# Performance work log

Measured on AMD Instinct MI355X. Metric: run time of the kernel, lower is better.

The kernel has to match this reference:

```python
import jax, jax.numpy as jnp
import numpy as np

N, DIM, DK, DV = 8192, 512, 128, 128


def setup_inputs() -> dict:
    key = jax.random.key(0)
    ks = jax.random.split(key, 6)
    s = lambda d: 1.0 / np.sqrt(d)
    return {
        "x": jax.random.normal(ks[0], (N, DIM), jnp.float32),
        "W": jax.random.normal(ks[1], (DK, DIM), jnp.float32) * s(DIM),
        "b": jax.random.normal(ks[2], (DK,), jnp.float32) * s(DIM),
        "Wv": jax.random.normal(ks[3], (DV, DIM), jnp.float32) * s(DIM),
        "bv": jax.random.normal(ks[4], (DV,), jnp.float32) * s(DIM),
        "a": jax.random.normal(ks[5], (2 * DK,), jnp.float32),
    }


def reference(x, W, b, Wv, bv, a):
    dk = a.shape[0] // 2
    wx = x @ W.T + b                      # [n, dk]
    # additive GAT score decomposed into two matvecs + outer sum
    s_src = wx @ a[:dk]                   # [n]
    s_dst = wx @ a[dk:]                   # [n]
    score = s_src[:, None] + s_dst[None, :]  # [n, n]
    score = jax.nn.leaky_relu(score, negative_slope=0.01)
    score = jax.nn.softmax(score, axis=-1)
    v = x @ Wv.T + bv                     # [n, dv]
    return score @ v                      # [n, dv]
```

## Files before the change

kernel.cpp:

```cpp
#include <hip/hip_runtime.h>
#include <math.h>

static constexpr int N    = 8192;
static constexpr int DIM  = 512;
static constexpr int DK   = 128;
static constexpr int DV   = 128;
static constexpr float SLOPE = 0.01f;

static constexpr int NCH  = 512;
static constexpr int CHSZ = 16;
static constexpr int NCOL = 258;

static constexpr int MT  = 128;
static constexpr int BK  = 32;
static constexpr int LDT = 132;

__global__ __launch_bounds__(256) void k_front(const float* __restrict__ x,
                                               const float* __restrict__ W,
                                               const float* __restrict__ b,
                                               const float* __restrict__ a,
                                               float* __restrict__ s_src,
                                               float* __restrict__ s_dst) {
    __shared__ float sa[2 * DK];
    __shared__ float sus[DIM + 32], sud[DIM + 32];
    __shared__ float sc[2];
    int tid = threadIdx.x;
    sa[tid] = a[tid];
    __syncthreads();

    {
        float p = 0.0f;
        if (tid < 64)        p = b[tid] * sa[tid] + b[tid + 64] * sa[tid + 64];
        else if (tid < 128) { int l = tid - 64; p = b[l] * sa[DK + l] + b[l + 64] * sa[DK + 64 + l]; }
#pragma unroll
        for (int off = 32; off > 0; off >>= 1) p += __shfl_down(p, off);
        if (tid == 0)  sc[0] = p;
        if (tid == 64) sc[1] = p;
    }

#pragma unroll
    for (int half = 0; half < 2; ++half) {
        int d = tid + half * 256;
        float us = 0.0f, ud = 0.0f;
#pragma unroll 4
        for (int k = 0; k < DK; ++k) {
            float w = W[(size_t)k * DIM + d];
            us += w * sa[k];
            ud += w * sa[DK + k];
        }
        int dp = d + (d >> 6) * 4;
        sus[dp] = us;
        sud[dp] = ud;
    }
    __syncthreads();

    int r   = tid >> 3;
    int seg = tid & 7;
    int row = blockIdx.x * 32 + r;
    const float* xr = x + (size_t)row * DIM;
    int base  = seg * 64;
    int baseP = base + seg * 4;
    float accs = 0.0f, accd = 0.0f;
#pragma unroll
    for (int i = 0; i < 16; ++i) {
        float4 q  = *reinterpret_cast<const float4*>(xr + base + i * 4);
        float4 u4 = *reinterpret_cast<const float4*>(&sus[baseP + i * 4]);
        float4 w4 = *reinterpret_cast<const float4*>(&sud[baseP + i * 4]);
        accs += q.x * u4.x + q.y * u4.y + q.z * u4.z + q.w * u4.w;
        accd += q.x * w4.x + q.y * w4.y + q.z * w4.z + q.w * w4.w;
    }
#pragma unroll
    for (int off = 4; off > 0; off >>= 1) {
        accs += __shfl_down(accs, off);
        accd += __shfl_down(accd, off);
    }
    if (seg == 0) {
        s_src[row] = accs + sc[0];
        s_dst[row] = accd + sc[1];
    }
}

__global__ __launch_bounds__(256) void k_v(const float* __restrict__ x,
                                           const float* __restrict__ Wv,
                                           float* __restrict__ vpart, int ksplit) {
    __shared__ float At[BK][LDT];
    __shared__ float Bt[BK][LDT];
    int tid = threadIdx.x;
    int mt  = blockIdx.x & 63;
    int ks  = blockIdx.x >> 6;
    int row0 = mt * MT;
    int ksub = DIM / ksplit;
    int kb0  = ks * ksub;
    int nt   = ksub / BK;
    int tx = tid & 15, ty = tid >> 4;

    float acc[8][8];
#pragma unroll
    for (int i = 0; i < 8; ++i)
#pragma unroll
        for (int j = 0; j < 8; ++j) acc[i][j] = 0.0f;

    int fr[4], fk[4];
#pragma unroll
    for (int i = 0; i < 4; ++i) {
        int f = tid + i * 256;
        fr[i] = f >> 3;
        fk[i] = (f & 7) * 4;
    }
    float4 px[4], pw[4];
#pragma unroll
    for (int i = 0; i < 4; ++i) {
        px[i] = *reinterpret_cast<const float4*>(x  + (size_t)(row0 + fr[i]) * DIM + kb0 + fk[i]);
        pw[i] = *reinterpret_cast<const float4*>(Wv + (size_t)fr[i] * DIM + kb0 + fk[i]);
    }

    for (int t = 0; t < nt; ++t) {
#pragma unroll
        for (int i = 0; i < 4; ++i) {
            At[fk[i] + 0][fr[i]] = px[i].x;
            At[fk[i] + 1][fr[i]] = px[i].y;
            At[fk[i] + 2][fr[i]] = px[i].z;
            At[fk[i] + 3][fr[i]] = px[i].w;
            Bt[fk[i] + 0][fr[i]] = pw[i].x;
            Bt[fk[i] + 1][fr[i]] = pw[i].y;
            Bt[fk[i] + 2][fr[i]] = pw[i].z;
            Bt[fk[i] + 3][fr[i]] = pw[i].w;
        }
        __syncthreads();
        if (t < nt - 1) {
            int kb = kb0 + (t + 1) * BK;
#pragma unroll
            for (int i = 0; i < 4; ++i) {
                px[i] = *reinterpret_cast<const float4*>(x  + (size_t)(row0 + fr[i]) * DIM + kb + fk[i]);
                pw[i] = *reinterpret_cast<const float4*>(Wv + (size_t)fr[i] * DIM + kb + fk[i]);
            }
        }
#pragma unroll 4
        for (int kk = 0; kk < BK; ++kk) {
            float4 a0 = *reinterpret_cast<const float4*>(&At[kk][ty * 4]);
            float4 a1 = *reinterpret_cast<const float4*>(&At[kk][64 + ty * 4]);
            float4 b0 = *reinterpret_cast<const float4*>(&Bt[kk][tx * 4]);
            float4 b1 = *reinterpret_cast<const float4*>(&Bt[kk][64 + tx * 4]);
            float av[8] = {a0.x, a0.y, a0.z, a0.w, a1.x, a1.y, a1.z, a1.w};
            float bw[8] = {b0.x, b0.y, b0.z, b0.w, b1.x, b1.y, b1.z, b1.w};
#pragma unroll
            for (int i = 0; i < 8; ++i)
#pragma unroll
                for (int j = 0; j < 8; ++j) acc[i][j] += av[i] * bw[j];
        }
        __syncthreads();
    }

#pragma unroll
    for (int rh = 0; rh < 2; ++rh)
#pragma unroll
        for (int i = 0; i < 4; ++i) {
            int row = row0 + rh * 64 + ty * 4 + i;
            float* dst = vpart + ((size_t)ks * N + row) * DV;
#pragma unroll
            for (int ch = 0; ch < 2; ++ch) {
                float4 o;
                o.x = acc[rh * 4 + i][ch * 4 + 0];
                o.y = acc[rh * 4 + i][ch * 4 + 1];
                o.z = acc[rh * 4 + i][ch * 4 + 2];
                o.w = acc[rh * 4 + i][ch * 4 + 3];
                *reinterpret_cast<float4*>(dst + ch * 64 + tx * 4) = o;
            }
        }
}

__global__ __launch_bounds__(256) void k_rank_scatter(const float* __restrict__ s_dst,
                                                      float* __restrict__ d_sorted,
                                                      int* __restrict__ perm) {
    __shared__ __align__(16) float sd[N];
    __shared__ int part[256];
    int tid = threadIdx.x;
    for (int t = tid; t < N / 4; t += 256)
        reinterpret_cast<float4*>(sd)[t] = reinterpret_cast<const float4*>(s_dst)[t];
    __syncthreads();
    int j0  = blockIdx.x * 16;
    int jj  = tid >> 4;
    int seg = tid & 15;
    int j   = j0 + jj;
    float dj = sd[j];
    int cnt = 0;
    const float4* sdv = reinterpret_cast<const float4*>(sd);
    for (int c = 0; c < 128; ++c) {
        int f4 = c * 16 + seg;
        float4 q = sdv[f4];
        int i0 = f4 * 4;
        cnt += (q.x < dj || (q.x == dj && (i0 + 0) < j));
        cnt += (q.y < dj || (q.y == dj && (i0 + 1) < j));
        cnt += (q.z < dj || (q.z == dj && (i0 + 2) < j));
        cnt += (q.w < dj || (q.w == dj && (i0 + 3) < j));
    }
    part[tid] = cnt;
    __syncthreads();
    if (tid < 16) {
        int s = 0;
#pragma unroll
        for (int t = 0; t < 16; ++t) s += part[tid * 16 + t];
        int jw = j0 + tid;
        d_sorted[s] = sd[jw];
        perm[s] = jw;
    }
}

__global__ __launch_bounds__(256) void k_vredY(const float* __restrict__ vpart,
                                               const float* __restrict__ bv,
                                               const float* __restrict__ d_sorted,
                                               const int* __restrict__ perm,
                                               float* __restrict__ Y1,
                                               float* __restrict__ Y2,
                                               double* __restrict__ chunk_tot,
                                               int ksplit) {
    __shared__ float sv[CHSZ][DV];
    __shared__ float se1[CHSZ], se2[CHSZ];
    int ch  = blockIdx.x;
    int tid = threadIdx.x;
    int g   = tid >> 5;
    int c4  = tid & 31;
    float dmax = d_sorted[N - 1];
    if (tid < CHSZ) {
        float d = d_sorted[ch * CHSZ + tid];
        se1[tid] = expf(d - dmax);
        se2[tid] = expf(SLOPE * d);
    }
    __syncthreads();
    float4 bb = reinterpret_cast<const float4*>(bv)[c4];
#pragma unroll
    for (int half = 0; half < 2; ++half) {
        int rl = half * 8 + g;
        int r  = ch * CHSZ + rl;
        int j  = perm[r];
        float4 s = {0.f, 0.f, 0.f, 0.f};
        for (int ksp = 0; ksp < ksplit; ++ksp) {
            float4 q = *reinterpret_cast<const float4*>(vpart + ((size_t)ksp * N + j) * DV + c4 * 4);
            s.x += q.x; s.y += q.y; s.z += q.z; s.w += q.w;
        }
        s.x += bb.x; s.y += bb.y; s.z += bb.z; s.w += bb.w;
        *reinterpret_cast<float4*>(&sv[rl][c4 * 4]) = s;
        float e1 = se1[rl], e2 = se2[rl];
        float4 o1 = {e1 * s.x, e1 * s.y, e1 * s.z, e1 * s.w};
        float4 o2 = {e2 * s.x, e2 * s.y, e2 * s.z, e2 * s.w};
        *reinterpret_cast<float4*>(Y1 + (size_t)r * DV + c4 * 4) = o1;
        *reinterpret_cast<float4*>(Y2 + (size_t)r * DV + c4 * 4) = o2;
    }
    __syncthreads();
    int col = tid & 127;
    bool is2 = tid >= 128;
    double acc = 0.0;
#pragma unroll
    for (int k = 0; k < CHSZ; ++k) {
        float e = is2 ? se2[k] : se1[k];
        acc += (double)(e * sv[k][col]);
    }
    chunk_tot[(size_t)ch * NCOL + tid] = acc;
    if (tid == 0) {
        double z = 0.0;
#pragma unroll
        for (int k = 0; k < CHSZ; ++k) z += (double)se1[k];
        chunk_tot[(size_t)ch * NCOL + 256] = z;
    }
    if (tid == 1) {
        double z = 0.0;
#pragma unroll
        for (int k = 0; k < CHSZ; ++k) z += (double)se2[k];
        chunk_tot[(size_t)ch * NCOL + 257] = z;
    }
}

__global__ __launch_bounds__(256) void k_coff(const double* __restrict__ chunk_tot,
                                              double* __restrict__ chunk_off,
                                              double* __restrict__ totals) {
    __shared__ double sp[256];
    int col = blockIdx.x;
    int tid = threadIdx.x;
    double v0 = chunk_tot[(size_t)(2 * tid) * NCOL + col];
    double v1 = chunk_tot[(size_t)(2 * tid + 1) * NCOL + col];
    double p = v0 + v1;
    sp[tid] = p;
    __syncthreads();
    for (int off = 1; off < 256; off <<= 1) {
        double t = (tid >= off) ? sp[tid - off] : 0.0;
        __syncthreads();
        sp[tid] += t;
        __syncthreads();
    }
    double excl = sp[tid] - p;
    chunk_off[(size_t)(2 * tid) * NCOL + col]     = excl;
    chunk_off[(size_t)(2 * tid + 1) * NCOL + col] = excl + v0;
    if (tid == 255) totals[col] = sp[255];
}

__global__ __launch_bounds__(256) void k_scanW(const float* __restrict__ Y1,
                                               const float* __restrict__ Y2,
                                               const float* __restrict__ d_sorted,
                                               const double* __restrict__ chunk_off,
                                               float* __restrict__ P1,
                                               float* __restrict__ P2,
                                               double* __restrict__ pz1,
                                               double* __restrict__ pz2) {
    int ch  = blockIdx.x;
    int tid = threadIdx.x;
    int col = tid & 127;
    bool is2 = tid >= 128;
    const float* Y = is2 ? Y2 : Y1;
    float* P       = is2 ? P2 : P1;
    double acc = chunk_off[(size_t)ch * NCOL + tid];
#pragma unroll
    for (int k = 0; k < CHSZ; ++k) {
        size_t idx = (size_t)(ch * CHSZ + k) * DV + col;
        P[idx] = (float)acc;
        acc += (double)Y[idx];
    }
    if (tid < 2) {
        float dmax = d_sorted[N - 1];
        double z = chunk_off[(size_t)ch * NCOL + 256 + tid];
        double* pz = tid == 0 ? pz1 : pz2;
#pragma unroll
        for (int k = 0; k < CHSZ; ++k) {
            int r = ch * CHSZ + k;
            float d = d_sorted[r];
            float e = (tid == 0) ? expf(d - dmax) : expf(SLOPE * d);
            pz[r] = z;
            z += (double)e;
        }
    }
}

__global__ __launch_bounds__(256) void k_final(const float* __restrict__ s_src,
                                               const float* __restrict__ d_sorted,
                                               const float* __restrict__ P1,
                                               const float* __restrict__ P2,
                                               const double* __restrict__ pz1,
                                               const double* __restrict__ pz2,
                                               const double* __restrict__ totals,
                                               float* __restrict__ out) {
    __shared__ int ski[8];
    __shared__ float ssi[8];
    int tid = threadIdx.x;
    int rbase = blockIdx.x * 8;
    if (tid < 8) {
        int row = rbase + tid;
        float si = s_src[row];
        float thr = -si;
        int lo = 0, hi = N;
        while (lo < hi) {
            int mid = (lo + hi) >> 1;
            if (d_sorted[mid] <= thr) lo = mid + 1; else hi = mid;
        }
        ski[tid] = lo;
        ssi[tid] = si;
    }
    __syncthreads();
    float dmax = d_sorted[N - 1];
    int dv = tid & 127;
    int half = tid >> 7;
    double T1 = totals[dv];
    double T2 = totals[128 + dv];
    double z1T = totals[256], z2T = totals[257];
#pragma unroll
    for (int it = 0; it < 4; ++it) {
        int r2 = it * 2 + half;
        int row = rbase + r2;
        float si = ssi[r2];
        int ki = ski[r2];
        float t = si + dmax;
        float m = t > 0.0f ? t : SLOPE * t;
        float alpha = expf(t - m);
        float beta  = expf(SLOPE * si - m);
        double suf1, sufz1, pre2, prez2;
        if (ki < N) {
            suf1  = T1 - (double)P1[(size_t)ki * DV + dv];
            sufz1 = z1T - pz1[ki];
            pre2  = (double)P2[(size_t)ki * DV + dv];
            prez2 = pz2[ki];
        } else {
            suf1 = 0.0; sufz1 = 0.0; pre2 = T2; prez2 = z2T;
        }
        double num = (double)alpha * suf1  + (double)beta * pre2;
        double den = (double)alpha * sufz1 + (double)beta * prez2;
        out[(size_t)row * DV + dv] = (float)(num / den);
    }
}

extern "C" void kernel_launch(void* const* d_in, const int* in_sizes, int n_in,
                              void* d_out, int out_size, void* d_ws, size_t ws_size,
                              hipStream_t stream) {
    const float* x  = (const float*)d_in[0];
    const float* W  = (const float*)d_in[1];
    const float* b  = (const float*)d_in[2];
    const float* Wv = (const float*)d_in[3];
    const float* bv = (const float*)d_in[4];
    const float* a  = (const float*)d_in[5];
    float* out = (float*)d_out;

    char* base = (char*)d_ws;
    size_t off = 0;
    auto carve = [&](size_t bytes) -> void* {
        void* p = base + off;
        off = (off + bytes + 255) & ~(size_t)255;
        return p;
    };
    float*  s_src     = (float*)carve(N * sizeof(float));
    float*  s_dst     = (float*)carve(N * sizeof(float));
    float*  d_sorted  = (float*)carve(N * sizeof(float));
    int*    perm      = (int*)carve(N * sizeof(int));
    double* pz1       = (double*)carve(N * sizeof(double));
    double* pz2       = (double*)carve(N * sizeof(double));
    double* chunk_tot = (double*)carve((size_t)NCH * NCOL * sizeof(double));
    double* chunk_off = (double*)carve((size_t)NCH * NCOL * sizeof(double));
    double* totals    = (double*)carve(NCOL * sizeof(double));
    float*  Y1        = (float*)carve((size_t)N * DV * sizeof(float));
    float*  Y2        = (float*)carve((size_t)N * DV * sizeof(float));

    const size_t planeB = (size_t)N * DV * sizeof(float);
    size_t avail = ws_size > off ? ws_size - off : 0;
    int ksplit = 2;
    if (avail >= 8 * planeB + 4096)      ksplit = 8;
    else if (avail >= 4 * planeB + 4096) ksplit = 4;
    if (ksplit == 8) ksplit = 4;
    size_t unionBytes = (size_t)(ksplit > 2 ? ksplit : 2) * planeB;
    char* uni = (char*)carve(unionBytes);
    float* vpart = (float*)uni;
    float* P1    = (float*)uni;
    float* P2    = (float*)(uni + planeB);

    k_front<<<N / 32, 256, 0, stream>>>(x, W, b, a, s_src, s_dst);
    k_v<<<64 * ksplit, 256, 0, stream>>>(x, Wv, vpart, ksplit);
    k_rank_scatter<<<N / 16, 256, 0, stream>>>(s_dst, d_sorted, perm);
    k_vredY<<<NCH, 256, 0, stream>>>(vpart, bv, d_sorted, perm, Y1, Y2, chunk_tot, ksplit);
    k_coff<<<NCOL, 256, 0, stream>>>(chunk_tot, chunk_off, totals);
    k_scanW<<<NCH, 256, 0, stream>>>(Y1, Y2, d_sorted, chunk_off, P1, P2, pz1, pz2);
    k_final<<<N / 8, 256, 0, stream>>>(s_src, d_sorted, P1, P2, pz1, pz2, totals, out);
}
```

Measured before the change: 160.1 us.

## Fuse score front-end with V GEMM and recompute V gather instead of storing Y planes

Merges the score-projection kernel and the split-K V GEMM into one launch whose blocks branch by index, so the two independent stages share the GPU. It also drops the Y1/Y2 intermediate planes: the scan kernel re-gathers and reduces vpart for each chunk and applies the exp weights itself, instead of reading stored weighted values. This removes one launch and two full N×DV write-and-read passes, at the cost of gathering and reducing vpart twice and a larger shared-memory footprint in the fused kernel.

```diff
diff --git a/kernel.cpp b/kernel.cpp
--- a/kernel.cpp
+++ b/kernel.cpp
@@ -14,6 +14,175 @@
 static constexpr int MT  = 128;
 static constexpr int BK  = 32;
 static constexpr int LDT = 132;
+static constexpr int KSPLIT = 4;
+static constexpr int KSUB   = DIM / KSPLIT;
+
+__device__ __forceinline__ void gemm_body(int mt, int ks, int ksub, int tid,
+                                          const float* __restrict__ x,
+                                          const float* __restrict__ Wv,
+                                          float* __restrict__ vpart,
+                                          float (*At)[LDT], float (*Bt)[LDT]) {
+    int row0 = mt * MT;
+    int kb0  = ks * ksub;
+    int nt   = ksub / BK;
+    int tx = tid & 15, ty = tid >> 4;
+
+    float acc[8][8];
+#pragma unroll
+    for (int i = 0; i < 8; ++i)
+#pragma unroll
+        for (int j = 0; j < 8; ++j) acc[i][j] = 0.0f;
+
+    int fr[4], fk[4];
+#pragma unroll
+    for (int i = 0; i < 4; ++i) {
+        int f = tid + i * 256;
+        fr[i] = f >> 3;
+        fk[i] = (f & 7) * 4;
+    }
+    float4 px[4], pw[4];
+#pragma unroll
+    for (int i = 0; i < 4; ++i) {
+        px[i] = *reinterpret_cast<const float4*>(x  + (size_t)(row0 + fr[i]) * DIM + kb0 + fk[i]);
+        pw[i] = *reinterpret_cast<const float4*>(Wv + (size_t)fr[i] * DIM + kb0 + fk[i]);
+    }
+
+    for (int t = 0; t < nt; ++t) {
+#pragma unroll
+        for (int i = 0; i < 4; ++i) {
+            At[fk[i] + 0][fr[i]] = px[i].x;
+            At[fk[i] + 1][fr[i]] = px[i].y;
+            At[fk[i] + 2][fr[i]] = px[i].z;
+            At[fk[i] + 3][fr[i]] = px[i].w;
+            Bt[fk[i] + 0][fr[i]] = pw[i].x;
+            Bt[fk[i] + 1][fr[i]] = pw[i].y;
+            Bt[fk[i] + 2][fr[i]] = pw[i].z;
+            Bt[fk[i] + 3][fr[i]] = pw[i].w;
+        }
+        __syncthreads();
+        if (t < nt - 1) {
+            int kb = kb0 + (t + 1) * BK;
+#pragma unroll
+            for (int i = 0; i < 4; ++i) {
+                px[i] = *reinterpret_cast<const float4*>(x  + (size_t)(row0 + fr[i]) * DIM + kb + fk[i]);
+                pw[i] = *reinterpret_cast<const float4*>(Wv + (size_t)fr[i] * DIM + kb + fk[i]);
+            }
+        }
+#pragma unroll 4
+        for (int kk = 0; kk < BK; ++kk) {
+            float4 a0 = *reinterpret_cast<const float4*>(&At[kk][ty * 4]);
+            float4 a1 = *reinterpret_cast<const float4*>(&At[kk][64 + ty * 4]);
+            float4 b0 = *reinterpret_cast<const float4*>(&Bt[kk][tx * 4]);
+            float4 b1 = *reinterpret_cast<const float4*>(&Bt[kk][64 + tx * 4]);
+            float av[8] = {a0.x, a0.y, a0.z, a0.w, a1.x, a1.y, a1.z, a1.w};
+            float bw[8] = {b0.x, b0.y, b0.z, b0.w, b1.x, b1.y, b1.z, b1.w};
+#pragma unroll
+            for (int i = 0; i < 8; ++i)
+#pragma unroll
+                for (int j = 0; j < 8; ++j) acc[i][j] += av[i] * bw[j];
+        }
+        __syncthreads();
+    }
+
+#pragma unroll
+    for (int rh = 0; rh < 2; ++rh)
+#pragma unroll
+        for (int i = 0; i < 4; ++i) {
+            int row = row0 + rh * 64 + ty * 4 + i;
+            float* dst = vpart + ((size_t)ks * N + row) * DV;
+#pragma unroll
+            for (int ch = 0; ch < 2; ++ch) {
+                float4 o;
+                o.x = acc[rh * 4 + i][ch * 4 + 0];
+                o.y = acc[rh * 4 + i][ch * 4 + 1];
+                o.z = acc[rh * 4 + i][ch * 4 + 2];
+                o.w = acc[rh * 4 + i][ch * 4 + 3];
+                *reinterpret_cast<float4*>(dst + ch * 64 + tx * 4) = o;
+            }
+        }
+}
+
+__device__ __forceinline__ void front_body(int fb, int tid,
+                                           const float* __restrict__ x,
+                                           const float* __restrict__ W,
+                                           const float* __restrict__ b,
+                                           const float* __restrict__ a,
+                                           float* __restrict__ s_src,
+                                           float* __restrict__ s_dst,
+                                           float* sa, float* sus, float* sud, float* sc) {
+    sa[tid] = a[tid];
+    __syncthreads();
+    {
+        float p = 0.0f;
+        if (tid < 64)        p = b[tid] * sa[tid] + b[tid + 64] * sa[tid + 64];
+        else if (tid < 128) { int l = tid - 64; p = b[l] * sa[DK + l] + b[l + 64] * sa[DK + 64 + l]; }
+#pragma unroll
+        for (int off = 32; off > 0; off >>= 1) p += __shfl_down(p, off);
+        if (tid == 0)  sc[0] = p;
+        if (tid == 64) sc[1] = p;
+    }
+#pragma unroll
+    for (int half = 0; half < 2; ++half) {
+        int d = tid + half * 256;
+        float us = 0.0f, ud = 0.0f;
+#pragma unroll 4
+        for (int k = 0; k < DK; ++k) {
+            float w = W[(size_t)k * DIM + d];
+            us += w * sa[k];
+            ud += w * sa[DK + k];
+        }
+        int dp = d + (d >> 6) * 4;
+        sus[dp] = us;
+        sud[dp] = ud;
+    }
+    __syncthreads();
+    int r   = tid >> 3;
+    int seg = tid & 7;
+    int row = fb * 32 + r;
+    const float* xr = x + (size_t)row * DIM;
+    int base  = seg * 64;
+    int baseP = base + seg * 4;
+    float accs = 0.0f, accd = 0.0f;
+#pragma unroll
+    for (int i = 0; i < 16; ++i) {
+        float4 q  = *reinterpret_cast<const float4*>(xr + base + i * 4);
+        float4 u4 = *reinterpret_cast<const float4*>(&sus[baseP + i * 4]);
+        float4 w4 = *reinterpret_cast<const float4*>(&sud[baseP + i * 4]);
+        accs += q.x * u4.x + q.y * u4.y + q.z * u4.z + q.w * u4.w;
+        accd += q.x * w4.x + q.y * w4.y + q.z * w4.z + q.w * w4.w;
+    }
+#pragma unroll
+    for (int off = 4; off > 0; off >>= 1) {
+        accs += __shfl_down(accs, off);
+        accd += __shfl_down(accd, off);
+    }
+    if (seg == 0) {
+        s_src[row] = accs + sc[0];
+        s_dst[row] = accd + sc[1];
+    }
+}
+
+__global__ __launch_bounds__(256) void k_frontv(const float* __restrict__ x,
+                                                const float* __restrict__ W,
+                                                const float* __restrict__ b,
+                                                const float* __restrict__ a,
+                                                const float* __restrict__ Wv,
+                                                float* __restrict__ s_src,
+                                                float* __restrict__ s_dst,
+                                                float* __restrict__ vpart) {
+    __shared__ float At[BK][LDT];
+    __shared__ float Bt[BK][LDT];
+    __shared__ float sa[2 * DK];
+    __shared__ float sus[DIM + 32], sud[DIM + 32];
+    __shared__ float sc[2];
+    int blk = blockIdx.x;
+    int tid = threadIdx.x;
+    if (blk < 256) {
+        gemm_body(blk & 63, blk >> 6, KSUB, tid, x, Wv, vpart, At, Bt);
+    } else {
+        front_body(blk - 256, tid, x, W, b, a, s_src, s_dst, sa, sus, sud, sc);
+    }
+}
 
 __global__ __launch_bounds__(256) void k_front(const float* __restrict__ x,
                                                const float* __restrict__ W,
@@ -24,60 +193,7 @@
     __shared__ float sa[2 * DK];
     __shared__ float sus[DIM + 32], sud[DIM + 32];
     __shared__ float sc[2];
-    int tid = threadIdx.x;
-    sa[tid] = a[tid];
-    __syncthreads();
-
-    {
-        float p = 0.0f;
-        if (tid < 64)        p = b[tid] * sa[tid] + b[tid + 64] * sa[tid + 64];
-        else if (tid < 128) { int l = tid - 64; p = b[l] * sa[DK + l] + b[l + 64] * sa[DK + 64 + l]; }
-#pragma unroll
-        for (int off = 32; off > 0; off >>= 1) p += __shfl_down(p, off);
-        if (tid == 0)  sc[0] = p;
-        if (tid == 64) sc[1] = p;
-    }
-
-#pragma unroll
-    for (int half = 0; half < 2; ++half) {
-        int d = tid + half * 256;
-        float us = 0.0f, ud = 0.0f;
-#pragma unroll 4
-        for (int k = 0; k < DK; ++k) {
-            float w = W[(size_t)k * DIM + d];
-            us += w * sa[k];
-            ud += w * sa[DK + k];
-        }
-        int dp = d + (d >> 6) * 4;
-        sus[dp] = us;
-        sud[dp] = ud;
-    }
-    __syncthreads();
-
-    int r   = tid >> 3;
-    int seg = tid & 7;
-    int row = blockIdx.x * 32 + r;
-    const float* xr = x + (size_t)row * DIM;
-    int base  = seg * 64;
-    int baseP = base + seg * 4;
-    float accs = 0.0f, accd = 0.0f;
-#pragma unroll
-    for (int i = 0; i < 16; ++i) {
-        float4 q  = *reinterpret_cast<const float4*>(xr + base + i * 4);
-        float4 u4 = *reinterpret_cast<const float4*>(&sus[baseP + i * 4]);
-        float4 w4 = *reinterpret_cast<const float4*>(&sud[baseP + i * 4]);
-        accs += q.x * u4.x + q.y * u4.y + q.z * u4.z + q.w * u4.w;
-        accd += q.x * w4.x + q.y * w4.y + q.z * w4.z + q.w * w4.w;
-    }
-#pragma unroll
-    for (int off = 4; off > 0; off >>= 1) {
-        accs += __shfl_down(accs, off);
-        accd += __shfl_down(accd, off);
-    }
-    if (seg == 0) {
-        s_src[row] = accs + sc[0];
-        s_dst[row] = accd + sc[1];
-    }
+    front_body(blockIdx.x, threadIdx.x, x, W, b, a, s_src, s_dst, sa, sus, sud, sc);
 }
 
 __global__ __launch_bounds__(256) void k_v(const float* __restrict__ x,
@@ -85,88 +201,7 @@
                                            float* __restrict__ vpart, int ksplit) {
     __shared__ float At[BK][LDT];
     __shared__ float Bt[BK][LDT];
-    int tid = threadIdx.x;
-    int mt  = blockIdx.x & 63;
-    int ks  = blockIdx.x >> 6;
-    int row0 = mt * MT;
-    int ksub = DIM / ksplit;
-    int kb0  = ks * ksub;
-    int nt   = ksub / BK;
-    int tx = tid & 15, ty = tid >> 4;
-
-    float acc[8][8];
-#pragma unroll
-    for (int i = 0; i < 8; ++i)
-#pragma unroll
-        for (int j = 0; j < 8; ++j) acc[i][j] = 0.0f;
-
-    int fr[4], fk[4];
-#pragma unroll
-    for (int i = 0; i < 4; ++i) {
-        int f = tid + i * 256;
-        fr[i] = f >> 3;
-        fk[i] = (f & 7) * 4;
-    }
-    float4 px[4], pw[4];
-#pragma unroll
-    for (int i = 0; i < 4; ++i) {
-        px[i] = *reinterpret_cast<const float4*>(x  + (size_t)(row0 + fr[i]) * DIM + kb0 + fk[i]);
-        pw[i] = *reinterpret_cast<const float4*>(Wv + (size_t)fr[i] * DIM + kb0 + fk[i]);
-    }
-
-    for (int t = 0; t < nt; ++t) {
-#pragma unroll
-        for (int i = 0; i < 4; ++i) {
-            At[fk[i] + 0][fr[i]] = px[i].x;
-            At[fk[i] + 1][fr[i]] = px[i].y;
-            At[fk[i] + 2][fr[i]] = px[i].z;
-            At[fk[i] + 3][fr[i]] = px[i].w;
-            Bt[fk[i] + 0][fr[i]] = pw[i].x;
-            Bt[fk[i] + 1][fr[i]] = pw[i].y;
-            Bt[fk[i] + 2][fr[i]] = pw[i].z;
-            Bt[fk[i] + 3][fr[i]] = pw[i].w;
-        }
-        __syncthreads();
-        if (t < nt - 1) {
-            int kb = kb0 + (t + 1) * BK;
-#pragma unroll
-            for (int i = 0; i < 4; ++i) {
-                px[i] = *reinterpret_cast<const float4*>(x  + (size_t)(row0 + fr[i]) * DIM + kb + fk[i]);
-                pw[i] = *reinterpret_cast<const float4*>(Wv + (size_t)fr[i] * DIM + kb + fk[i]);
-            }
-        }
-#pragma unroll 4
-        for (int kk = 0; kk < BK; ++kk) {
-            float4 a0 = *reinterpret_cast<const float4*>(&At[kk][ty * 4]);
-            float4 a1 = *reinterpret_cast<const float4*>(&At[kk][64 + ty * 4]);
-            float4 b0 = *reinterpret_cast<const float4*>(&Bt[kk][tx * 4]);
-            float4 b1 = *reinterpret_cast<const float4*>(&Bt[kk][64 + tx * 4]);
-            float av[8] = {a0.x, a0.y, a0.z, a0.w, a1.x, a1.y, a1.z, a1.w};
-            float bw[8] = {b0.x, b0.y, b0.z, b0.w, b1.x, b1.y, b1.z, b1.w};
-#pragma unroll
-            for (int i = 0; i < 8; ++i)
-#pragma unroll
-                for (int j = 0; j < 8; ++j) acc[i][j] += av[i] * bw[j];
-        }
-        __syncthreads();
-    }
-
-#pragma unroll
-    for (int rh = 0; rh < 2; ++rh)
-#pragma unroll
-        for (int i = 0; i < 4; ++i) {
-            int row = row0 + rh * 64 + ty * 4 + i;
-            float* dst = vpart + ((size_t)ks * N + row) * DV;
-#pragma unroll
-            for (int ch = 0; ch < 2; ++ch) {
-                float4 o;
-                o.x = acc[rh * 4 + i][ch * 4 + 0];
-                o.y = acc[rh * 4 + i][ch * 4 + 1];
-                o.z = acc[rh * 4 + i][ch * 4 + 2];
-                o.w = acc[rh * 4 + i][ch * 4 + 3];
-                *reinterpret_cast<float4*>(dst + ch * 64 + tx * 4) = o;
-            }
-        }
+    gemm_body(blockIdx.x & 63, blockIdx.x >> 6, DIM / ksplit, threadIdx.x, x, Wv, vpart, At, Bt);
 }
 
 __global__ __launch_bounds__(256) void k_rank_scatter(const float* __restrict__ s_dst,
@@ -206,20 +241,12 @@
     }
 }
 
-__global__ __launch_bounds__(256) void k_vredY(const float* __restrict__ vpart,
-                                               const float* __restrict__ bv,
-                                               const float* __restrict__ d_sorted,
-                                               const int* __restrict__ perm,
-                                               float* __restrict__ Y1,
-                                               float* __restrict__ Y2,
-                                               double* __restrict__ chunk_tot,
-                                               int ksplit) {
-    __shared__ float sv[CHSZ][DV];
-    __shared__ float se1[CHSZ], se2[CHSZ];
-    int ch  = blockIdx.x;
-    int tid = threadIdx.x;
-    int g   = tid >> 5;
-    int c4  = tid & 31;
+__device__ __forceinline__ void gather_chunk(int ch, int tid, int ksplit,
+                                             const float* __restrict__ vpart,
+                                             const float* __restrict__ bv,
+                                             const float* __restrict__ d_sorted,
+                                             const int* __restrict__ perm,
+                                             float (*sv)[DV], float* se1, float* se2) {
     float dmax = d_sorted[N - 1];
     if (tid < CHSZ) {
         float d = d_sorted[ch * CHSZ + tid];
@@ -227,6 +254,8 @@
         se2[tid] = expf(SLOPE * d);
     }
     __syncthreads();
+    int g  = tid >> 5;
+    int c4 = tid & 31;
     float4 bb = reinterpret_cast<const float4*>(bv)[c4];
 #pragma unroll
     for (int half = 0; half < 2; ++half) {
@@ -240,13 +269,21 @@
         }
         s.x += bb.x; s.y += bb.y; s.z += bb.z; s.w += bb.w;
         *reinterpret_cast<float4*>(&sv[rl][c4 * 4]) = s;
-        float e1 = se1[rl], e2 = se2[rl];
-        float4 o1 = {e1 * s.x, e1 * s.y, e1 * s.z, e1 * s.w};
-        float4 o2 = {e2 * s.x, e2 * s.y, e2 * s.z, e2 * s.w};
-        *reinterpret_cast<float4*>(Y1 + (size_t)r * DV + c4 * 4) = o1;
-        *reinterpret_cast<float4*>(Y2 + (size_t)r * DV + c4 * 4) = o2;
-    }
-    __syncthreads();
+    }
+    __syncthreads();
+}
+
+__global__ __launch_bounds__(256) void k_vredT(const float* __restrict__ vpart,
+                                               const float* __restrict__ bv,
+                                               const float* __restrict__ d_sorted,
+                                               const int* __restrict__ perm,
+                                               double* __restrict__ chunk_tot,
+                                               int ksplit) {
+    __shared__ float sv[CHSZ][DV];
+    __shared__ float se1[CHSZ], se2[CHSZ];
+    int ch  = blockIdx.x;
+    int tid = threadIdx.x;
+    gather_chunk(ch, tid, ksplit, vpart, bv, d_sorted, perm, sv, se1, se2);
     int col = tid & 127;
     bool is2 = tid >= 128;
     double acc = 0.0;
@@ -293,38 +330,39 @@
     if (tid == 255) totals[col] = sp[255];
 }
 
-__global__ __launch_bounds__(256) void k_scanW(const float* __restrict__ Y1,
-                                               const float* __restrict__ Y2,
-                                               const float* __restrict__ d_sorted,
-                                               const double* __restrict__ chunk_off,
-                                               float* __restrict__ P1,
-                                               float* __restrict__ P2,
-                                               double* __restrict__ pz1,
-                                               double* __restrict__ pz2) {
+__global__ __launch_bounds__(256) void k_scanW2(const float* __restrict__ vpart,
+                                                const float* __restrict__ bv,
+                                                const float* __restrict__ d_sorted,
+                                                const int* __restrict__ perm,
+                                                const double* __restrict__ chunk_off,
+                                                float* __restrict__ P1,
+                                                float* __restrict__ P2,
+                                                double* __restrict__ pz1,
+                                                double* __restrict__ pz2,
+                                                int ksplit) {
+    __shared__ float sv[CHSZ][DV];
+    __shared__ float se1[CHSZ], se2[CHSZ];
     int ch  = blockIdx.x;
     int tid = threadIdx.x;
+    gather_chunk(ch, tid, ksplit, vpart, bv, d_sorted, perm, sv, se1, se2);
     int col = tid & 127;
     bool is2 = tid >= 128;
-    const float* Y = is2 ? Y2 : Y1;
-    float* P       = is2 ? P2 : P1;
+    const float* se = is2 ? se2 : se1;
+    float* P        = is2 ? P2  : P1;
     double acc = chunk_off[(size_t)ch * NCOL + tid];
 #pragma unroll
     for (int k = 0; k < CHSZ; ++k) {
-        size_t idx = (size_t)(ch * CHSZ + k) * DV + col;
-        P[idx] = (float)acc;
-        acc += (double)Y[idx];
+        P[(size_t)(ch * CHSZ + k) * DV + col] = (float)acc;
+        acc += (double)(se[k] * sv[k][col]);
     }
     if (tid < 2) {
-        float dmax = d_sorted[N - 1];
         double z = chunk_off[(size_t)ch * NCOL + 256 + tid];
-        double* pz = tid == 0 ? pz1 : pz2;
+        const float* sez = (tid == 0) ? se1 : se2;
+        double* pz = (tid == 0) ? pz1 : pz2;
 #pragma unroll
         for (int k = 0; k < CHSZ; ++k) {
-            int r = ch * CHSZ + k;
-            float d = d_sorted[r];
-            float e = (tid == 0) ? expf(d - dmax) : expf(SLOPE * d);
-            pz[r] = z;
-            z += (double)e;
+            pz[ch * CHSZ + k] = z;
+            z += (double)sez[k];
         }
     }
 }
@@ -412,26 +450,24 @@
     double* chunk_tot = (double*)carve((size_t)NCH * NCOL * sizeof(double));
     double* chunk_off = (double*)carve((size_t)NCH * NCOL * sizeof(double));
     double* totals    = (double*)carve(NCOL * sizeof(double));
-    float*  Y1        = (float*)carve((size_t)N * DV * sizeof(float));
-    float*  Y2        = (float*)carve((size_t)N * DV * sizeof(float));
 
     const size_t planeB = (size_t)N * DV * sizeof(float);
     size_t avail = ws_size > off ? ws_size - off : 0;
-    int ksplit = 2;
-    if (avail >= 8 * planeB + 4096)      ksplit = 8;
-    else if (avail >= 4 * planeB + 4096) ksplit = 4;
-    if (ksplit == 8) ksplit = 4;
-    size_t unionBytes = (size_t)(ksplit > 2 ? ksplit : 2) * planeB;
-    char* uni = (char*)carve(unionBytes);
-    float* vpart = (float*)uni;
-    float* P1    = (float*)uni;
-    float* P2    = (float*)(uni + planeB);
-
-    k_front<<<N / 32, 256, 0, stream>>>(x, W, b, a, s_src, s_dst);
-    k_v<<<64 * ksplit, 256, 0, stream>>>(x, Wv, vpart, ksplit);
+    bool fused = avail >= 6 * planeB + 4096;
+    int ksplit = fused ? KSPLIT : 2;
+    float* vpart = (float*)carve((size_t)ksplit * planeB);
+    float* P1    = (float*)carve(planeB);
+    float* P2    = (float*)carve(planeB);
+
+    if (fused) {
+        k_frontv<<<512, 256, 0, stream>>>(x, W, b, a, Wv, s_src, s_dst, vpart);
+    } else {
+        k_front<<<N / 32, 256, 0, stream>>>(x, W, b, a, s_src, s_dst);
+        k_v<<<64 * ksplit, 256, 0, stream>>>(x, Wv, vpart, ksplit);
+    }
     k_rank_scatter<<<N / 16, 256, 0, stream>>>(s_dst, d_sorted, perm);
-    k_vredY<<<NCH, 256, 0, stream>>>(vpart, bv, d_sorted, perm, Y1, Y2, chunk_tot, ksplit);
+    k_vredT<<<NCH, 256, 0, stream>>>(vpart, bv, d_sorted, perm, chunk_tot, ksplit);
     k_coff<<<NCOL, 256, 0, stream>>>(chunk_tot, chunk_off, totals);
-    k_scanW<<<NCH, 256, 0, stream>>>(Y1, Y2, d_sorted, chunk_off, P1, P2, pz1, pz2);
+    k_scanW2<<<NCH, 256, 0, stream>>>(vpart, bv, d_sorted, perm, chunk_off, P1, P2, pz1, pz2, ksplit);
     k_final<<<N / 8, 256, 0, stream>>>(s_src, d_sorted, P1, P2, pz1, pz2, totals, out);
 }
```

Measured after the change: 139.3 us. 1.15x faster.
